# Kernel optimization log

Measured on AMD Instinct MI355X. Metric: run time of the kernel, lower is better.

Reference implementation:

```python
import jax, jax.numpy as jnp
import numpy as np

N_WIRES = 14
N_LAYERS = 3
DIM = 2 ** N_WIRES
BATCH = 1024


def _rx(theta):
    # RX(t) = [[cos t/2, -i sin t/2], [-i sin t/2, cos t/2]]
    c = jnp.cos(theta / 2).astype(jnp.complex64)
    s = jnp.sin(theta / 2).astype(jnp.complex64)
    return jnp.stack([jnp.stack([c, -1j * s]), jnp.stack([-1j * s, c])])


def _ry(theta):
    # RY(t) = [[cos t/2, -sin t/2], [sin t/2, cos t/2]]
    c = jnp.cos(theta / 2).astype(jnp.complex64)
    s = jnp.sin(theta / 2).astype(jnp.complex64)
    return jnp.stack([jnp.stack([c, -s]), jnp.stack([s, c])])


def _apply_1q(psi, U, w):
    # psi: (B, 2, 2, ..., 2); apply 2x2 U on qubit axis w+1
    psi = jnp.tensordot(psi, U, axes=((w + 1,), (1,)))  # contracted axis moves to end
    return jnp.moveaxis(psi, -1, w + 1)


def _apply_cnot(psi, c, t):
    # control qubit c, target qubit t (Python ints)
    a0 = jax.lax.index_in_dim(psi, 0, axis=c + 1, keepdims=True)
    a1 = jax.lax.index_in_dim(psi, 1, axis=c + 1, keepdims=True)
    a1 = jnp.flip(a1, axis=t + 1)  # X on target within control=1 subspace
    return jnp.concatenate([a0, a1], axis=c + 1)


def _circuit_features(state, params):
    # state: (B, 2**n) real normalized amplitudes -> PauliZ expvals (B, n)
    n = N_WIRES
    psi = state.astype(jnp.complex64).reshape((-1,) + (2,) * n)
    for layer in range(N_LAYERS):
        for w in range(n):
            psi = _apply_1q(psi, _rx(params[layer, w, 0]), w)
            psi = _apply_1q(psi, _ry(params[layer, w, 1]), w)
        for w in range(n - 1):
            psi = _apply_cnot(psi, w, w + 1)
        psi = _apply_cnot(psi, n - 1, 0)
    probs = jnp.real(psi * jnp.conj(psi))  # (B, 2, ..., 2)
    feats = []
    for w in range(n):
        axes = tuple(a for a in range(1, n + 1) if a != w + 1)
        p = jnp.sum(probs, axis=axes)  # (B, 2)
        feats.append(p[:, 0] - p[:, 1])  # <Z_w>
    return jnp.stack(feats, axis=1)  # (B, n)


def setup_inputs() -> dict:
    key = jax.random.key(0)
    k1, k2, k3 = jax.random.split(key, 3)
    state = jax.random.normal(k1, (BATCH, DIM), dtype=jnp.float32)
    state = state / jnp.linalg.norm(state, axis=1, keepdims=True)  # valid statevectors
    params = jax.random.normal(k2, (N_LAYERS, N_WIRES, 2), dtype=jnp.float32)
    head_w = jax.random.normal(k3, (1, N_WIRES), dtype=jnp.float32) * (1.0 / np.sqrt(N_WIRES))
    head_b = jnp.zeros((1,), dtype=jnp.float32)
    return {"state": state, "params": params, "head_w": head_w, "head_b": head_b}


def reference(state, params, head_w, head_b):
    feats = _circuit_features(state, params)          # (B, n_wires)
    out = feats @ head_w.T + head_b                   # (B, 1)
    return out[:, 0]                                  # (B,)
```

## Files before the change

### kernel.cpp

```cpp
#include <hip/hip_runtime.h>
#include <utility>

#define NW 14
#define NL 3
#define DIM 16384
#define NG  (NL * NW)
#define TPB 1024
#define MAXSP 12

typedef float v2f __attribute__((ext_vector_type(2)));

struct SP {
    int J = 0, nr = 0, nl = 0;
    unsigned dirs[4]  = {};
    unsigned traw[10] = {};
    unsigned tR[10] = {}, tW[10] = {};
    unsigned sxR[16] = {}, sxW[16] = {};
    unsigned pv[8]   = {};
    unsigned cpar[8] = {};
    unsigned gid[8]  = {};
    int wflag = 1;
};
struct Sched2 {
    int nsp = 0;
    SP sp[MAXSP] = {};
    unsigned stA[10] = {};
    unsigned stK[4]  = {};
    unsigned pz[NW]  = {};
    unsigned nib[NW] = {};
    int ok = 1;
};

constexpr unsigned fap(const unsigned* g, unsigned x) {
    unsigned r = 0;
    for (int b = 4; b < 14; ++b) if ((x >> b) & 1u) r ^= g[b - 4];
    return x ^ r;
}
constexpr int rank4n(const unsigned* v) {
    unsigned bas[4] = {}; int nb = 0;
    for (int i = 0; i < 4; ++i) {
        unsigned r = v[i] & 15u;
        for (int j = 0; j < nb; ++j) {
            int hb = 3; while (hb > 0 && !((bas[j] >> hb) & 1u)) --hb;
            if ((r >> hb) & 1u) r ^= bas[j];
        }
        if (r) bas[nb++] = r;
    }
    return nb;
}

constexpr Sched2 build2() {
    Sched2 S{};
    unsigned mk[NG] = {}, vmg[NG] = {}, zm[NW] = {};
    {
        unsigned A[NW] = {};
        for (int w = 0; w < NW; ++w) A[w] = 1u << (NW - 1 - w);
        int g = 0;
        for (int l = 0; l < NL; ++l) {
            unsigned rows[NW] = {};
            for (int u = 0; u < NW; ++u) rows[u] = A[u] | (1u << (NW + u));
            for (int col = 0; col < NW; ++col) {
                int piv = col;
                while (piv < NW && !((rows[piv] >> col) & 1u)) ++piv;
                if (piv >= NW) { S.ok = 0; continue; }
                unsigned tmp = rows[col]; rows[col] = rows[piv]; rows[piv] = tmp;
                for (int r = 0; r < NW; ++r)
                    if (r != col && ((rows[r] >> col) & 1u)) rows[r] ^= rows[col];
            }
            for (int w = 0; w < NW; ++w) {
                unsigned m = 0;
                for (int r = 0; r < NW; ++r) m |= ((rows[r] >> (NW + w)) & 1u) << r;
                mk[g] = m; vmg[g] = A[w]; ++g;
            }
            for (int w = 0; w < NW - 1; ++w) A[w + 1] ^= A[w];
            A[0] ^= A[NW - 1];
        }
        for (int w = 0; w < NW; ++w) zm[w] = A[w];
    }
    int gs = 0;
    while (gs < NG && S.nsp < MAXSP) {
        SP& P = S.sp[S.nsp];
        unsigned bas[14] = {}; int nb = 0;
        int j = gs;
        while (j < NG && (j - gs) < 8) {
            unsigned r = mk[j];
            for (int i = 0; i < nb; ++i) {
                int hb = 13; while (hb > 0 && !((bas[i] >> hb) & 1u)) --hb;
                if ((r >> hb) & 1u) r ^= bas[i];
            }
            if (!r) break;
            bas[nb++] = r; ++j;
        }
        P.J = j - gs; P.nr = P.J < 4 ? P.J : 4; P.nl = P.J - P.nr;
        for (int q = 0; q < P.J; ++q) P.gid[q] = (unsigned)(gs + q);
        for (int q = 0; q < P.nr; ++q) P.dirs[q] = mk[gs + q];
        for (int q = P.nr; q < 4; ++q) {
            for (int b = 0; b < NW; ++b) {
                unsigned r = 1u << b;
                for (int i = 0; i < nb; ++i) {
                    int hb = 13; while (hb > 0 && !((bas[i] >> hb) & 1u)) --hb;
                    if ((r >> hb) & 1u) r ^= bas[i];
                }
                if (r) { bas[nb++] = r; P.dirs[q] = 1u << b; break; }
            }
        }
        unsigned lm[4] = {};
        for (int i = 0; i < P.nl; ++i) lm[i] = mk[gs + 4 + i];
        unsigned tt[4] = { 0, 0, 0, 0 };
        if (P.nl > 0) tt[0] = lm[0];
        if (P.nl > 1) tt[1] = lm[1];
        if (P.nl > 2) tt[2] = lm[2] ^ tt[0] ^ tt[1];
        if (P.nl > 3) tt[3] = lm[3] ^ lm[2];
        for (int i = P.nl; i < 4; ++i) {
            for (int b = 0; b < NW; ++b) {
                unsigned r = 1u << b;
                for (int k2 = 0; k2 < nb; ++k2) {
                    int hb = 13; while (hb > 0 && !((bas[k2] >> hb) & 1u)) --hb;
                    if ((r >> hb) & 1u) r ^= bas[k2];
                }
                if (r) { bas[nb++] = r; tt[i] = 1u << b; break; }
            }
        }
        for (int i = 0; i < 4; ++i) P.traw[i] = tt[i];
        for (int b6 = 4; b6 < 10; ++b6) {
            for (int b = 0; b < NW; ++b) {
                unsigned r = 1u << b;
                for (int k2 = 0; k2 < nb; ++k2) {
                    int hb = 13; while (hb > 0 && !((bas[k2] >> hb) & 1u)) --hb;
                    if ((r >> hb) & 1u) r ^= bas[k2];
                }
                if (r) { bas[nb++] = r; P.traw[b6] = 1u << b; break; }
            }
        }
        if (nb != 14) S.ok = 0;
        for (int q = 0; q < P.J; ++q) {
            unsigned vm = vmg[gs + q], p = 0;
            for (int b = 0; b < 10; ++b)
                if (__builtin_popcount(P.traw[b] & vm) & 1) p |= 1u << b;
            P.pv[q] = p;
            unsigned cp = 0;
            for (int s = 0; s < 16; ++s) {
                unsigned sx = 0;
                for (int q2 = 0; q2 < 4; ++q2) if ((s >> q2) & 1) sx ^= P.dirs[q2];
                if (__builtin_popcount(sx & vm) & 1) cp |= 1u << s;
            }
            P.cpar[q] = cp;
        }
        ++S.nsp; gs = j;
    }
    if (gs < NG) S.ok = 0;
    S.sp[S.nsp - 1].wflag = 0;
    for (int t = 0; t < S.nsp; ++t) {
        unsigned wd[4] = {}, rd[4] = {};
        if (t == 0) { wd[0] = 4; wd[1] = 8; wd[2] = 16; wd[3] = 32; }
        else for (int i = 0; i < 4; ++i) wd[i] = S.sp[t - 1].traw[i];
        for (int i = 0; i < 4; ++i) rd[i] = S.sp[t].traw[i];
        unsigned bg[10] = {}; int bscore = -1;
        for (unsigned seed = 0; seed < 512u; ++seed) {
            unsigned g[10] = {};
            if (seed) {
                for (int b = 0; b < 10; ++b) {
                    unsigned h = (seed * 2654435761u) ^ ((unsigned)(b + 3) * 0x9E3779B9u);
                    h ^= h >> 16; h *= 2246822519u; h ^= h >> 13;
                    g[b] = h & 15u;
                }
            }
            unsigned W[4] = {}, R[4] = {};
            for (int i = 0; i < 4; ++i) { W[i] = fap(g, wd[i]); R[i] = fap(g, rd[i]); }
            int sc = rank4n(W) + rank4n(R);
            if (sc > bscore) {
                bscore = sc;
                for (int b = 0; b < 10; ++b) bg[b] = g[b];
                if (sc == 8) break;
            }
        }
        for (int b = 0; b < 10; ++b) S.sp[t].tR[b] = fap(bg, S.sp[t].traw[b]);
        for (int s = 0; s < 16; ++s) {
            unsigned sx = 0;
            for (int q = 0; q < 4; ++q) if ((s >> q) & 1) sx ^= S.sp[t].dirs[q];
            S.sp[t].sxR[s] = fap(bg, sx);
        }
        if (t == 0) {
            for (int b = 0; b < 10; ++b) S.stA[b] = fap(bg, 4u << b);
            for (int k = 0; k < 4; ++k) S.stK[k] = fap(bg, (unsigned)k << 12);
        } else {
            for (int b = 0; b < 10; ++b) S.sp[t - 1].tW[b] = fap(bg, S.sp[t - 1].traw[b]);
            for (int s = 0; s < 16; ++s) {
                unsigned sx = 0;
                for (int q = 0; q < 4; ++q) if ((s >> q) & 1) sx ^= S.sp[t - 1].dirs[q];
                S.sp[t - 1].sxW[s] = fap(bg, sx);
            }
        }
    }
    for (int w = 0; w < NW; ++w) {
        const SP& L = S.sp[S.nsp - 1];
        unsigned p = 0;
        for (int b = 0; b < 10; ++b)
            if (__builtin_popcount(L.traw[b] & zm[w]) & 1) p |= 1u << b;
        S.pz[w] = p;
        unsigned nv = 0;
        for (int q = 0; q < 4; ++q)
            if (__builtin_popcount(L.dirs[q] & zm[w]) & 1) nv |= 1u << q;
        S.nib[w] = nv;
    }
    return S;
}
constexpr Sched2 SC2 = build2();
static_assert(SC2.ok == 1, "schedule build failed");
static_assert(SC2.nsp <= MAXSP, "too many superphases");

template<class F, unsigned... I>
__device__ __forceinline__ void static_for_impl(F&& f, std::integer_sequence<unsigned, I...>) {
    (f(std::integral_constant<unsigned, I>{}), ...);
}
template<unsigned N, class F>
__device__ __forceinline__ void static_for(F&& f) {
    static_for_impl(static_cast<F&&>(f), std::make_integer_sequence<unsigned, N>{});
}

template<int NEGLO, int NEGHI>
__device__ __forceinline__ v2f cmul(v2f k, v2f x) {
    v2f y;
    if constexpr (!NEGLO)
        asm("v_pk_mul_f32 %0, %1, %2 op_sel:[0,0] op_sel_hi:[0,1]"
            : "=&v"(y) : "v"(k), "v"(x));
    else
        asm("v_pk_mul_f32 %0, %1, %2 op_sel:[0,0] op_sel_hi:[0,1] neg_lo:[1,0] neg_hi:[1,0]"
            : "=&v"(y) : "v"(k), "v"(x));
    if constexpr (!NEGHI)
        asm("v_pk_fma_f32 %0, %1, %2, %0 op_sel:[1,1,0] op_sel_hi:[1,0,1] neg_lo:[0,1,0]"
            : "+v"(y) : "v"(k), "v"(x));
    else
        asm("v_pk_fma_f32 %0, %1, %2, %0 op_sel:[1,1,0] op_sel_hi:[1,0,1] neg_lo:[1,1,0] neg_hi:[1,0,0]"
            : "+v"(y) : "v"(k), "v"(x));
    return y;
}
template<int NEGLO, int NEGHI>
__device__ __forceinline__ void cmac(v2f& y, v2f k, v2f x) {
    if constexpr (!NEGLO)
        asm("v_pk_fma_f32 %0, %1, %2, %0 op_sel:[0,0,0] op_sel_hi:[0,1,1]"
            : "+v"(y) : "v"(k), "v"(x));
    else
        asm("v_pk_fma_f32 %0, %1, %2, %0 op_sel:[0,0,0] op_sel_hi:[0,1,1] neg_lo:[1,0,0] neg_hi:[1,0,0]"
            : "+v"(y) : "v"(k), "v"(x));
    if constexpr (!NEGHI)
        asm("v_pk_fma_f32 %0, %1, %2, %0 op_sel:[1,1,0] op_sel_hi:[1,0,1] neg_lo:[0,1,0]"
            : "+v"(y) : "v"(k), "v"(x));
    else
        asm("v_pk_fma_f32 %0, %1, %2, %0 op_sel:[1,1,0] op_sel_hi:[1,0,1] neg_lo:[1,1,0] neg_hi:[1,0,0]"
            : "+v"(y) : "v"(k), "v"(x));
}
template<bool CS> __device__ __forceinline__ v2f  cmulA(v2f k, v2f x) { return cmul<0, CS ? 1 : 0>(k, x); }
template<bool CS> __device__ __forceinline__ void cmacB(v2f& y, v2f k, v2f x) { cmac<CS ? 1 : 0, 0>(y, k, x); }

constexpr int lane_ctrl(int li) {
    return li == 0 ? 0xB1 : li == 1 ? 0x4E : li == 2 ? 0x141 : 0x140;
}
template<int CTRL>
__device__ __forceinline__ v2f dppx(v2f x) {
    int lo = __builtin_amdgcn_update_dpp(0, __float_as_int(x.x), CTRL, 0xf, 0xf, false);
    int hi = __builtin_amdgcn_update_dpp(0, __float_as_int(x.y), CTRL, 0xf, 0xf, false);
    return (v2f){ __int_as_float(lo), __int_as_float(hi) };
}

template<int PIDX>
__device__ __forceinline__ void apply_sp(char* psiB, const float4* __restrict__ umat,
                                         unsigned tid, v2f* x)
{
    unsigned frep = 0;
    static_for<10>([&](auto Bc) {
        constexpr int b = (int)decltype(Bc)::value;
        constexpr unsigned mm = SC2.sp[PIDX].tR[b] |
                                (SC2.sp[PIDX].wflag ? (SC2.sp[PIDX].tW[b] << 16) : 0u);
        frep ^= mm & (unsigned)(-(int)((tid >> b) & 1u));
    });
    const unsigned srepR8 = (frep & 0x3FFFu) << 3;
    const unsigned srepW8 = ((frep >> 16) & 0x3FFFu) << 3;

    static_for<16>([&](auto Sc) {
        constexpr unsigned s = decltype(Sc)::value;
        constexpr unsigned off = SC2.sp[PIDX].sxR[s] << 3;
        x[s] = *(const v2f*)(psiB + (srepR8 ^ off));
    });
    if constexpr (SC2.sp[PIDX].wflag)
        __syncthreads();

    static_for<8>([&](auto Qc) {
        constexpr int q = (int)decltype(Qc)::value;
        if constexpr (q < SC2.sp[PIDX].J) {
            constexpr unsigned cp = SC2.sp[PIDX].cpar[q];
            constexpr unsigned pv = SC2.sp[PIDX].pv[q];
            const float4 u = umat[SC2.sp[PIDX].gid[q]];
            const unsigned sm = ((unsigned)__popc(tid & pv)) << 31;
            v2f A, B;
            A.x = u.x; A.y = __uint_as_float(__float_as_uint(u.y) ^ sm);
            B.x = __uint_as_float(__float_as_uint(u.z) ^ sm); B.y = u.w;
            if constexpr (q < SC2.sp[PIDX].nr) {
                static_for<8>([&](auto Pc) {
                    constexpr unsigned p    = decltype(Pc)::value;
                    constexpr unsigned lowm = (1u << q) - 1u;
                    constexpr unsigned s0   = ((p & ~lowm) << 1) | (p & lowm);
                    constexpr unsigned s1   = s0 | (1u << q);
                    constexpr bool c0 = (cp >> s0) & 1u;
                    constexpr bool c1 = (cp >> s1) & 1u;
                    const v2f x0 = x[s0], x1 = x[s1];
                    v2f y0 = cmulA<c0>(A, x0); cmacB<c0>(y0, B, x1);
                    v2f y1 = cmulA<c1>(A, x1); cmacB<c1>(y1, B, x0);
                    x[s0] = y0; x[s1] = y1;
                });
            } else {
                constexpr int ctrl = lane_ctrl(q - SC2.sp[PIDX].nr);
                static_for<16>([&](auto Sc) {
                    constexpr unsigned s = decltype(Sc)::value;
                    constexpr bool cs = (cp >> s) & 1u;
                    v2f recv = dppx<ctrl>(x[s]);
                    v2f y = cmulA<cs>(A, x[s]); cmacB<cs>(y, B, recv);
                    x[s] = y;
                });
            }
        }
    });

    if constexpr (SC2.sp[PIDX].wflag) {
        static_for<16>([&](auto Sc) {
            constexpr unsigned s = decltype(Sc)::value;
            constexpr unsigned off = SC2.sp[PIDX].sxW[s] << 3;
            *(v2f*)(psiB + (srepW8 ^ off)) = x[s];
        });
        __syncthreads();
    }
}

__global__ __launch_bounds__(TPB) void qsim_kernel(
    const float* __restrict__ state,
    const float* __restrict__ params,
    const float* __restrict__ head_w,
    const float* __restrict__ head_b,
    float* __restrict__ out)
{
    __shared__ v2f    psi[DIM];
    __shared__ float4 umat[NG];
    __shared__ float  red[TPB / 64];
    char* psiB = (char*)psi;
    const unsigned tid = threadIdx.x;

    if (tid < NG) {
        float t1 = 0.5f * params[2 * tid + 0];
        float t2 = 0.5f * params[2 * tid + 1];
        float s1, c1, s2, c2;
        sincosf(t1, &s1, &c1);
        sincosf(t2, &s2, &c2);
        umat[tid] = make_float4(c1 * c2, s1 * s2, -s2 * c1, -c2 * s1);
    }

    unsigned tpart = 0;
    static_for<10>([&](auto Bc) {
        constexpr int b = (int)decltype(Bc)::value;
        constexpr unsigned m = SC2.stA[b];
        tpart ^= m & (unsigned)(-(int)((tid >> b) & 1u));
    });
    const float4* st4 = reinterpret_cast<const float4*>(state) + (size_t)blockIdx.x * (DIM / 4);
    static_for<4>([&](auto Kc) {
        constexpr int k = (int)decltype(Kc)::value;
        float4 v = st4[tid + k * TPB];
        const unsigned bb = (tpart ^ SC2.stK[k]) << 3;
        *(v2f*)(psiB + (bb ^ (0u << 3))) = (v2f){ v.x, 0.f };
        *(v2f*)(psiB + (bb ^ (1u << 3))) = (v2f){ v.y, 0.f };
        *(v2f*)(psiB + (bb ^ (2u << 3))) = (v2f){ v.z, 0.f };
        *(v2f*)(psiB + (bb ^ (3u << 3))) = (v2f){ v.w, 0.f };
    });
    __syncthreads();

    v2f x[16];
    static_for<MAXSP>([&](auto Pc) {
        constexpr int p = (int)decltype(Pc)::value;
        if constexpr (p < SC2.nsp) apply_sp<p>(psiB, umat, tid, x);
    });

    float e[NW];
    static_for<NW>([&](auto Wc) {
        constexpr int w = (int)decltype(Wc)::value;
        constexpr unsigned pzw = SC2.pz[w];
        float hw = head_w[w];
        e[w] = (__popc(tid & pzw) & 1) ? -hw : hw;
    });
    float c[16];
    static_for<16>([&](auto Mc) { c[decltype(Mc)::value] = 0.f; });
    static_for<NW>([&](auto Wc) {
        constexpr int w = (int)decltype(Wc)::value;
        c[SC2.nib[w]] += e[w];
    });
    static_for<4>([&](auto Bc) {
        constexpr unsigned B = 1u << decltype(Bc)::value;
        static_for<16>([&](auto Kc) {
            constexpr unsigned k = decltype(Kc)::value;
            if constexpr (!(k & B)) {
                float a = c[k], b = c[k | B];
                c[k] = a + b; c[k | B] = a - b;
            }
        });
    });
    float acc = 0.f;
    static_for<16>([&](auto Sc) {
        constexpr int s = (int)decltype(Sc)::value;
        acc += (x[s].x * x[s].x + x[s].y * x[s].y) * c[s];
    });

#pragma unroll
    for (int off = 32; off > 0; off >>= 1)
        acc += __shfl_down(acc, off, 64);
    const unsigned lane = tid & 63, wv = tid >> 6;
    if (lane == 0) red[wv] = acc;
    __syncthreads();
    if (tid == 0) {
        float tot = 0.f;
#pragma unroll
        for (int i = 0; i < TPB / 64; ++i) tot += red[i];
        out[blockIdx.x] = tot + head_b[0];
    }
}

extern "C" void kernel_launch(void* const* d_in, const int* in_sizes, int n_in,
                              void* d_out, int out_size, void* d_ws, size_t ws_size,
                              hipStream_t stream) {
    const float* state  = (const float*)d_in[0];
    const float* params = (const float*)d_in[1];
    const float* head_w = (const float*)d_in[2];
    const float* head_b = (const float*)d_in[3];
    float* out = (float*)d_out;

    qsim_kernel<<<out_size, TPB, 0, stream>>>(state, params, head_w, head_b, out);
}
```

Before: 157.9 us.

## Replace superphase schedule with fixed 11-phase wave-private shared-memory permutation scheme

Rebuilds the compile-time schedule so each phase applies 4 gates in registers, with the basis split into 6 lane bits, 4 register bits and 4 fixed wave-local bits. The cross-lane DPP gate path is dropped. Reads use a simple contiguous per-wave address, and writes go through a computed XOR permutation. Because the fixed wave bits keep some phases' data inside a wave, barriers are only needed every other phase, cutting __syncthreads count. In exchange it runs more phases with more shared-memory round trips, and the write pattern may cause LDS bank conflicts.

```diff
diff --git a/kernel.cpp b/kernel.cpp
--- a/kernel.cpp
+++ b/kernel.cpp
@@ -6,51 +6,60 @@
 #define DIM 16384
 #define NG  (NL * NW)
 #define TPB 1024
-#define MAXSP 12
+#define NPH3 11
 
 typedef float v2f __attribute__((ext_vector_type(2)));
 
-struct SP {
-    int J = 0, nr = 0, nl = 0;
-    unsigned dirs[4]  = {};
-    unsigned traw[10] = {};
-    unsigned tR[10] = {}, tW[10] = {};
-    unsigned sxR[16] = {}, sxW[16] = {};
-    unsigned pv[8]   = {};
-    unsigned cpar[8] = {};
-    unsigned gid[8]  = {};
-    int wflag = 1;
+struct S3 {
+    int ok = 1;
+    unsigned Lane[NPH3][6] = {};
+    unsigned Reg[NPH3][4]  = {};
+    unsigned Vw[4]         = {};
+    unsigned WT[NPH3][6]   = {};
+    unsigned WS[NPH3][16]  = {};
+    unsigned pv[NPH3][4]   = {};
+    unsigned cp[NPH3][4]   = {};
+    unsigned ST[10] = {}, STK[4] = {}, STJ[4] = {};
+    unsigned pz[NW] = {}, nib[NW] = {};
 };
-struct Sched2 {
-    int nsp = 0;
-    SP sp[MAXSP] = {};
-    unsigned stA[10] = {};
-    unsigned stK[4]  = {};
-    unsigned pz[NW]  = {};
-    unsigned nib[NW] = {};
-    int ok = 1;
-};
-
-constexpr unsigned fap(const unsigned* g, unsigned x) {
-    unsigned r = 0;
-    for (int b = 4; b < 14; ++b) if ((x >> b) & 1u) r ^= g[b - 4];
-    return x ^ r;
-}
-constexpr int rank4n(const unsigned* v) {
-    unsigned bas[4] = {}; int nb = 0;
-    for (int i = 0; i < 4; ++i) {
-        unsigned r = v[i] & 15u;
-        for (int j = 0; j < nb; ++j) {
-            int hb = 3; while (hb > 0 && !((bas[j] >> hb) & 1u)) --hb;
-            if ((r >> hb) & 1u) r ^= bas[j];
-        }
-        if (r) bas[nb++] = r;
-    }
-    return nb;
-}
-
-constexpr Sched2 build2() {
-    Sched2 S{};
+
+constexpr int rank14(const unsigned* v, int n) {
+    unsigned piv[14] = {};
+    int r = 0;
+    for (int i = 0; i < n; ++i) {
+        unsigned x = v[i];
+        for (int bit = 13; bit >= 0; --bit) {
+            if (!((x >> bit) & 1u)) continue;
+            if (piv[bit]) { x ^= piv[bit]; }
+            else { piv[bit] = x; ++r; x = 0; break; }
+        }
+    }
+    return r;
+}
+
+constexpr unsigned coords14(const unsigned bas[14], unsigned v, int& ok) {
+    unsigned pv14[14] = {}, pc14[14] = {};
+    for (int b = 0; b < 14; ++b) {
+        unsigned x = bas[b], c = 1u << b;
+        for (int bit = 13; bit >= 0; --bit) {
+            if (!((x >> bit) & 1u)) continue;
+            if (pv14[bit]) { x ^= pv14[bit]; c ^= pc14[bit]; }
+            else { pv14[bit] = x; pc14[bit] = c; x = 0; break; }
+        }
+        if (x) ok = 0;
+    }
+    unsigned x = v, c = 0;
+    for (int bit = 13; bit >= 0; --bit) {
+        if ((x >> bit) & 1u) {
+            if (!pv14[bit]) { ok = 0; return 0; }
+            x ^= pv14[bit]; c ^= pc14[bit];
+        }
+    }
+    return c;
+}
+
+constexpr S3 build3() {
+    S3 S{};
     unsigned mk[NG] = {}, vmg[NG] = {}, zm[NW] = {};
     {
         unsigned A[NW] = {};
@@ -77,137 +86,173 @@
         }
         for (int w = 0; w < NW; ++w) zm[w] = A[w];
     }
-    int gs = 0;
-    while (gs < NG && S.nsp < MAXSP) {
-        SP& P = S.sp[S.nsp];
+    for (int p = 0; p < NPH3; ++p) {
+        int J = (p < 10) ? 4 : 2;
+        for (int q = 0; q < J; ++q) S.Reg[p][q] = mk[4 * p + q];
+    }
+    {
+        int found = 0;
+        for (unsigned seed = 1; seed < 256u && !found; ++seed) {
+            unsigned cand[4] = {};
+            for (int i = 0; i < 4; ++i) {
+                unsigned h = (seed * 2654435761u) ^ ((unsigned)(i + 1) * 0x9E3779B9u);
+                h ^= h >> 15; h *= 2246822519u; h ^= h >> 13; h *= 3266489917u; h ^= h >> 16;
+                cand[i] = h & 0x3FFFu;
+            }
+            if (rank14(cand, 4) != 4) continue;
+            int good = 1;
+            for (int g = 0; g < 6 && good; ++g) {
+                int nm = (g < 5) ? 8 : 2;
+                unsigned set[12] = {}; int n = 0;
+                for (int i = 0; i < nm; ++i) set[n++] = mk[8 * g + i];
+                for (int i = 0; i < 4; ++i) set[n++] = cand[i];
+                if (rank14(set, n) != n) good = 0;
+            }
+            if (good) { for (int i = 0; i < 4; ++i) S.Vw[i] = cand[i]; found = 1; }
+        }
+        if (!found) S.ok = 0;
+    }
+    for (int g = 0; g < 6; ++g) {
+        int nm = (g < 5) ? 8 : 2;
         unsigned bas[14] = {}; int nb = 0;
-        int j = gs;
-        while (j < NG && (j - gs) < 8) {
-            unsigned r = mk[j];
-            for (int i = 0; i < nb; ++i) {
-                int hb = 13; while (hb > 0 && !((bas[i] >> hb) & 1u)) --hb;
-                if ((r >> hb) & 1u) r ^= bas[i];
-            }
-            if (!r) break;
-            bas[nb++] = r; ++j;
-        }
-        P.J = j - gs; P.nr = P.J < 4 ? P.J : 4; P.nl = P.J - P.nr;
-        for (int q = 0; q < P.J; ++q) P.gid[q] = (unsigned)(gs + q);
-        for (int q = 0; q < P.nr; ++q) P.dirs[q] = mk[gs + q];
-        for (int q = P.nr; q < 4; ++q) {
-            for (int b = 0; b < NW; ++b) {
-                unsigned r = 1u << b;
-                for (int i = 0; i < nb; ++i) {
-                    int hb = 13; while (hb > 0 && !((bas[i] >> hb) & 1u)) --hb;
-                    if ((r >> hb) & 1u) r ^= bas[i];
+        for (int i = 0; i < 4; ++i) bas[nb++] = S.Vw[i];
+        for (int i = 0; i < nm; ++i) bas[nb++] = mk[8 * g + i];
+        unsigned fill[12] = {}; int nf = 0;
+        for (int b = 0; b < 14 && nb < 14; ++b) {
+            unsigned t[15] = {};
+            for (int i = 0; i < nb; ++i) t[i] = bas[i];
+            t[nb] = 1u << b;
+            if (rank14(t, nb + 1) == nb + 1) { bas[nb++] = 1u << b; fill[nf++] = 1u << b; }
+        }
+        if (nb != 14) S.ok = 0;
+        if (g < 5) {
+            int pA = 2 * g, pB = 2 * g + 1;
+            for (int b = 0; b < 4; ++b) { S.Lane[pA][b] = S.Reg[pB][b]; S.Lane[pB][b] = S.Reg[pA][b]; }
+            S.Lane[pA][4] = fill[0]; S.Lane[pA][5] = fill[1];
+            S.Lane[pB][4] = fill[0]; S.Lane[pB][5] = fill[1];
+        } else {
+            S.Reg[10][2] = fill[0]; S.Reg[10][3] = fill[1];
+            for (int b = 0; b < 6; ++b) S.Lane[10][b] = fill[2 + b];
+        }
+    }
+    for (int t = NPH3 - 2; t >= 0; --t) {
+        unsigned bas[14] = {};
+        for (int b = 0; b < 6; ++b) bas[b] = S.Lane[t + 1][b];
+        for (int q = 0; q < 4; ++q) bas[6 + q] = S.Reg[t + 1][q];
+        for (int j = 0; j < 4; ++j) bas[10 + j] = S.Vw[j];
+        unsigned rb[4] = {}; int rn = 0;
+        for (int b = 0; b < 6; ++b) {
+            int bestcs = 0, bestg = -1; unsigned bestr = 0;
+            for (int cs = 0; cs < 16; ++cs) {
+                unsigned c = 0;
+                for (int q = 0; q < 4; ++q) if ((cs >> q) & 1) c ^= S.Reg[t][q];
+                int ok2 = 1;
+                unsigned r = coords14(bas, S.Lane[t][b] ^ c, ok2) & 15u;
+                if (!ok2) continue;
+                unsigned x = r;
+                for (int i = 0; i < rn; ++i) {
+                    int hb = 3; while (hb > 0 && !((rb[i] >> hb) & 1u)) --hb;
+                    if ((x >> hb) & 1u) x ^= rb[i];
                 }
-                if (r) { bas[nb++] = r; P.dirs[q] = 1u << b; break; }
-            }
-        }
-        unsigned lm[4] = {};
-        for (int i = 0; i < P.nl; ++i) lm[i] = mk[gs + 4 + i];
-        unsigned tt[4] = { 0, 0, 0, 0 };
-        if (P.nl > 0) tt[0] = lm[0];
-        if (P.nl > 1) tt[1] = lm[1];
-        if (P.nl > 2) tt[2] = lm[2] ^ tt[0] ^ tt[1];
-        if (P.nl > 3) tt[3] = lm[3] ^ lm[2];
-        for (int i = P.nl; i < 4; ++i) {
-            for (int b = 0; b < NW; ++b) {
-                unsigned r = 1u << b;
-                for (int k2 = 0; k2 < nb; ++k2) {
-                    int hb = 13; while (hb > 0 && !((bas[k2] >> hb) & 1u)) --hb;
-                    if ((r >> hb) & 1u) r ^= bas[k2];
-                }
-                if (r) { bas[nb++] = r; tt[i] = 1u << b; break; }
-            }
-        }
-        for (int i = 0; i < 4; ++i) P.traw[i] = tt[i];
-        for (int b6 = 4; b6 < 10; ++b6) {
-            for (int b = 0; b < NW; ++b) {
-                unsigned r = 1u << b;
-                for (int k2 = 0; k2 < nb; ++k2) {
-                    int hb = 13; while (hb > 0 && !((bas[k2] >> hb) & 1u)) --hb;
-                    if ((r >> hb) & 1u) r ^= bas[k2];
-                }
-                if (r) { bas[nb++] = r; P.traw[b6] = 1u << b; break; }
-            }
-        }
-        if (nb != 14) S.ok = 0;
-        for (int q = 0; q < P.J; ++q) {
-            unsigned vm = vmg[gs + q], p = 0;
-            for (int b = 0; b < 10; ++b)
-                if (__builtin_popcount(P.traw[b] & vm) & 1) p |= 1u << b;
-            P.pv[q] = p;
-            unsigned cp = 0;
+                int gain = x ? 1 : 0;
+                if (gain > bestg) { bestg = gain; bestcs = cs; bestr = r; }
+                if (gain == 1) break;
+            }
+            unsigned c = 0;
+            for (int q = 0; q < 4; ++q) if ((bestcs >> q) & 1) c ^= S.Reg[t][q];
+            S.Lane[t][b] ^= c;
+            unsigned x = bestr;
+            for (int i = 0; i < rn; ++i) {
+                int hb = 3; while (hb > 0 && !((rb[i] >> hb) & 1u)) --hb;
+                if ((x >> hb) & 1u) x ^= rb[i];
+            }
+            if (x && rn < 4) rb[rn++] = x;
+        }
+        int okc = 1;
+        for (int b = 0; b < 6; ++b) S.WT[t][b] = coords14(bas, S.Lane[t][b], okc);
+        for (int s = 0; s < 16; ++s) {
+            unsigned v = 0;
+            for (int q = 0; q < 4; ++q) if ((s >> q) & 1) v ^= S.Reg[t][q];
+            S.WS[t][s] = coords14(bas, v, okc);
+        }
+        if (!okc) S.ok = 0;
+        if ((t & 1) == 0) {
+            for (int b = 0; b < 6; ++b) if (S.WT[t][b] >> 10) S.ok = 0;
+            for (int s = 0; s < 16; ++s) if (S.WS[t][s] >> 10) S.ok = 0;
+        }
+        for (int ub = 0; ub < 10; ++ub) {
+            unsigned wamp = (ub < 6) ? S.Lane[t][ub] : S.Vw[ub - 6];
+            unsigned widx = (ub < 6) ? S.WT[t][ub] : (1u << (10 + ub - 6));
+            unsigned ramp = 0;
+            for (int b = 0; b < 6; ++b) if ((widx >> b) & 1u) ramp ^= S.Lane[t + 1][b];
+            for (int q = 0; q < 4; ++q) if ((widx >> (6 + q)) & 1u) ramp ^= S.Reg[t + 1][q];
+            for (int j = 0; j < 4; ++j) if ((widx >> (10 + j)) & 1u) ramp ^= S.Vw[j];
+            if (ramp != wamp) S.ok = 0;
+        }
+        for (int q = 0; q < 4; ++q) {
+            unsigned widx = S.WS[t][1u << q];
+            unsigned ramp = 0;
+            for (int b = 0; b < 6; ++b) if ((widx >> b) & 1u) ramp ^= S.Lane[t + 1][b];
+            for (int qq = 0; qq < 4; ++qq) if ((widx >> (6 + qq)) & 1u) ramp ^= S.Reg[t + 1][qq];
+            for (int j = 0; j < 4; ++j) if ((widx >> (10 + j)) & 1u) ramp ^= S.Vw[j];
+            if (ramp != S.Reg[t][q]) S.ok = 0;
+        }
+    }
+    for (int p = 0; p < NPH3; ++p) {
+        int J = (p < 10) ? 4 : 2;
+        for (int q = 0; q < J; ++q) {
+            unsigned vm = vmg[4 * p + q], pvm = 0;
+            for (int b = 0; b < 6; ++b)
+                if (__builtin_popcount(S.Lane[p][b] & vm) & 1) pvm |= 1u << b;
+            for (int j = 0; j < 4; ++j)
+                if (__builtin_popcount(S.Vw[j] & vm) & 1) pvm |= 1u << (6 + j);
+            S.pv[p][q] = pvm;
+            unsigned cpm = 0;
             for (int s = 0; s < 16; ++s) {
-                unsigned sx = 0;
-                for (int q2 = 0; q2 < 4; ++q2) if ((s >> q2) & 1) sx ^= P.dirs[q2];
-                if (__builtin_popcount(sx & vm) & 1) cp |= 1u << s;
-            }
-            P.cpar[q] = cp;
-        }
-        ++S.nsp; gs = j;
-    }
-    if (gs < NG) S.ok = 0;
-    S.sp[S.nsp - 1].wflag = 0;
-    for (int t = 0; t < S.nsp; ++t) {
-        unsigned wd[4] = {}, rd[4] = {};
-        if (t == 0) { wd[0] = 4; wd[1] = 8; wd[2] = 16; wd[3] = 32; }
-        else for (int i = 0; i < 4; ++i) wd[i] = S.sp[t - 1].traw[i];
-        for (int i = 0; i < 4; ++i) rd[i] = S.sp[t].traw[i];
-        unsigned bg[10] = {}; int bscore = -1;
-        for (unsigned seed = 0; seed < 512u; ++seed) {
-            unsigned g[10] = {};
-            if (seed) {
-                for (int b = 0; b < 10; ++b) {
-                    unsigned h = (seed * 2654435761u) ^ ((unsigned)(b + 3) * 0x9E3779B9u);
-                    h ^= h >> 16; h *= 2246822519u; h ^= h >> 13;
-                    g[b] = h & 15u;
-                }
-            }
-            unsigned W[4] = {}, R[4] = {};
-            for (int i = 0; i < 4; ++i) { W[i] = fap(g, wd[i]); R[i] = fap(g, rd[i]); }
-            int sc = rank4n(W) + rank4n(R);
-            if (sc > bscore) {
-                bscore = sc;
-                for (int b = 0; b < 10; ++b) bg[b] = g[b];
-                if (sc == 8) break;
-            }
-        }
-        for (int b = 0; b < 10; ++b) S.sp[t].tR[b] = fap(bg, S.sp[t].traw[b]);
-        for (int s = 0; s < 16; ++s) {
-            unsigned sx = 0;
-            for (int q = 0; q < 4; ++q) if ((s >> q) & 1) sx ^= S.sp[t].dirs[q];
-            S.sp[t].sxR[s] = fap(bg, sx);
-        }
-        if (t == 0) {
-            for (int b = 0; b < 10; ++b) S.stA[b] = fap(bg, 4u << b);
-            for (int k = 0; k < 4; ++k) S.stK[k] = fap(bg, (unsigned)k << 12);
-        } else {
-            for (int b = 0; b < 10; ++b) S.sp[t - 1].tW[b] = fap(bg, S.sp[t - 1].traw[b]);
-            for (int s = 0; s < 16; ++s) {
-                unsigned sx = 0;
-                for (int q = 0; q < 4; ++q) if ((s >> q) & 1) sx ^= S.sp[t - 1].dirs[q];
-                S.sp[t - 1].sxW[s] = fap(bg, sx);
-            }
+                unsigned v = 0;
+                for (int q2 = 0; q2 < 4; ++q2) if ((s >> q2) & 1) v ^= S.Reg[p][q2];
+                if (__builtin_popcount(v & vm) & 1) cpm |= 1u << s;
+            }
+            S.cp[p][q] = cpm;
+        }
+    }
+    {
+        unsigned bas[14] = {};
+        for (int b = 0; b < 6; ++b) bas[b] = S.Lane[0][b];
+        for (int q = 0; q < 4; ++q) bas[6 + q] = S.Reg[0][q];
+        for (int j = 0; j < 4; ++j) bas[10 + j] = S.Vw[j];
+        int okc = 1;
+        for (int b = 0; b < 10; ++b) S.ST[b] = coords14(bas, 1u << (b + 2), okc);
+        for (int k = 0; k < 4; ++k) S.STK[k] = coords14(bas, (unsigned)k << 12, okc);
+        for (int j = 0; j < 4; ++j) S.STJ[j] = coords14(bas, (unsigned)j, okc);
+        if (!okc) S.ok = 0;
+        for (int ub = 0; ub < 18; ++ub) {
+            unsigned amp = (ub < 10) ? (1u << (ub + 2))
+                         : (ub < 14) ? ((unsigned)(ub - 10) << 12) : (unsigned)(ub - 14);
+            unsigned widx = (ub < 10) ? S.ST[ub] : (ub < 14) ? S.STK[ub - 10] : S.STJ[ub - 14];
+            unsigned ramp = 0;
+            for (int b = 0; b < 6; ++b) if ((widx >> b) & 1u) ramp ^= S.Lane[0][b];
+            for (int q = 0; q < 4; ++q) if ((widx >> (6 + q)) & 1u) ramp ^= S.Reg[0][q];
+            for (int j = 0; j < 4; ++j) if ((widx >> (10 + j)) & 1u) ramp ^= S.Vw[j];
+            if (ramp != amp) S.ok = 0;
         }
     }
     for (int w = 0; w < NW; ++w) {
-        const SP& L = S.sp[S.nsp - 1];
-        unsigned p = 0;
-        for (int b = 0; b < 10; ++b)
-            if (__builtin_popcount(L.traw[b] & zm[w]) & 1) p |= 1u << b;
-        S.pz[w] = p;
+        unsigned pzm = 0;
+        for (int b = 0; b < 6; ++b)
+            if (__builtin_popcount(S.Lane[10][b] & zm[w]) & 1) pzm |= 1u << b;
+        for (int j = 0; j < 4; ++j)
+            if (__builtin_popcount(S.Vw[j] & zm[w]) & 1) pzm |= 1u << (6 + j);
+        S.pz[w] = pzm;
         unsigned nv = 0;
         for (int q = 0; q < 4; ++q)
-            if (__builtin_popcount(L.dirs[q] & zm[w]) & 1) nv |= 1u << q;
+            if (__builtin_popcount(S.Reg[10][q] & zm[w]) & 1) nv |= 1u << q;
         S.nib[w] = nv;
     }
     return S;
 }
-constexpr Sched2 SC2 = build2();
-static_assert(SC2.ok == 1, "schedule build failed");
-static_assert(SC2.nsp <= MAXSP, "too many superphases");
+constexpr S3 SC3 = build3();
+static_assert(SC3.ok == 1, "schedule build failed");
 
 template<class F, unsigned... I>
 __device__ __forceinline__ void static_for_impl(F&& f, std::integer_sequence<unsigned, I...>) {
@@ -252,84 +297,6 @@
 }
 template<bool CS> __device__ __forceinline__ v2f  cmulA(v2f k, v2f x) { return cmul<0, CS ? 1 : 0>(k, x); }
 template<bool CS> __device__ __forceinline__ void cmacB(v2f& y, v2f k, v2f x) { cmac<CS ? 1 : 0, 0>(y, k, x); }
-
-constexpr int lane_ctrl(int li) {
-    return li == 0 ? 0xB1 : li == 1 ? 0x4E : li == 2 ? 0x141 : 0x140;
-}
-template<int CTRL>
-__device__ __forceinline__ v2f dppx(v2f x) {
-    int lo = __builtin_amdgcn_update_dpp(0, __float_as_int(x.x), CTRL, 0xf, 0xf, false);
-    int hi = __builtin_amdgcn_update_dpp(0, __float_as_int(x.y), CTRL, 0xf, 0xf, false);
-    return (v2f){ __int_as_float(lo), __int_as_float(hi) };
-}
-
-template<int PIDX>
-__device__ __forceinline__ void apply_sp(char* psiB, const float4* __restrict__ umat,
-                                         unsigned tid, v2f* x)
-{
-    unsigned frep = 0;
-    static_for<10>([&](auto Bc) {
-        constexpr int b = (int)decltype(Bc)::value;
-        constexpr unsigned mm = SC2.sp[PIDX].tR[b] |
-                                (SC2.sp[PIDX].wflag ? (SC2.sp[PIDX].tW[b] << 16) : 0u);
-        frep ^= mm & (unsigned)(-(int)((tid >> b) & 1u));
-    });
-    const unsigned srepR8 = (frep & 0x3FFFu) << 3;
-    const unsigned srepW8 = ((frep >> 16) & 0x3FFFu) << 3;
-
-    static_for<16>([&](auto Sc) {
-        constexpr unsigned s = decltype(Sc)::value;
-        constexpr unsigned off = SC2.sp[PIDX].sxR[s] << 3;
-        x[s] = *(const v2f*)(psiB + (srepR8 ^ off));
-    });
-    if constexpr (SC2.sp[PIDX].wflag)
-        __syncthreads();
-
-    static_for<8>([&](auto Qc) {
-        constexpr int q = (int)decltype(Qc)::value;
-        if constexpr (q < SC2.sp[PIDX].J) {
-            constexpr unsigned cp = SC2.sp[PIDX].cpar[q];
-            constexpr unsigned pv = SC2.sp[PIDX].pv[q];
-            const float4 u = umat[SC2.sp[PIDX].gid[q]];
-            const unsigned sm = ((unsigned)__popc(tid & pv)) << 31;
-            v2f A, B;
-            A.x = u.x; A.y = __uint_as_float(__float_as_uint(u.y) ^ sm);
-            B.x = __uint_as_float(__float_as_uint(u.z) ^ sm); B.y = u.w;
-            if constexpr (q < SC2.sp[PIDX].nr) {
-                static_for<8>([&](auto Pc) {
-                    constexpr unsigned p    = decltype(Pc)::value;
-                    constexpr unsigned lowm = (1u << q) - 1u;
-                    constexpr unsigned s0   = ((p & ~lowm) << 1) | (p & lowm);
-                    constexpr unsigned s1   = s0 | (1u << q);
-                    constexpr bool c0 = (cp >> s0) & 1u;
-                    constexpr bool c1 = (cp >> s1) & 1u;
-                    const v2f x0 = x[s0], x1 = x[s1];
-                    v2f y0 = cmulA<c0>(A, x0); cmacB<c0>(y0, B, x1);
-                    v2f y1 = cmulA<c1>(A, x1); cmacB<c1>(y1, B, x0);
-                    x[s0] = y0; x[s1] = y1;
-                });
-            } else {
-                constexpr int ctrl = lane_ctrl(q - SC2.sp[PIDX].nr);
-                static_for<16>([&](auto Sc) {
-                    constexpr unsigned s = decltype(Sc)::value;
-                    constexpr bool cs = (cp >> s) & 1u;
-                    v2f recv = dppx<ctrl>(x[s]);
-                    v2f y = cmulA<cs>(A, x[s]); cmacB<cs>(y, B, recv);
-                    x[s] = y;
-                });
-            }
-        }
-    });
-
-    if constexpr (SC2.sp[PIDX].wflag) {
-        static_for<16>([&](auto Sc) {
-            constexpr unsigned s = decltype(Sc)::value;
-            constexpr unsigned off = SC2.sp[PIDX].sxW[s] << 3;
-            *(v2f*)(psiB + (srepW8 ^ off)) = x[s];
-        });
-        __syncthreads();
-    }
-}
 
 __global__ __launch_bounds__(TPB) void qsim_kernel(
     const float* __restrict__ state,
@@ -353,34 +320,75 @@
         umat[tid] = make_float4(c1 * c2, s1 * s2, -s2 * c1, -c2 * s1);
     }
 
-    unsigned tpart = 0;
+    unsigned sidx = 0;
     static_for<10>([&](auto Bc) {
         constexpr int b = (int)decltype(Bc)::value;
-        constexpr unsigned m = SC2.stA[b];
-        tpart ^= m & (unsigned)(-(int)((tid >> b) & 1u));
+        sidx ^= SC3.ST[b] & (unsigned)(-(int)((tid >> b) & 1u));
     });
     const float4* st4 = reinterpret_cast<const float4*>(state) + (size_t)blockIdx.x * (DIM / 4);
     static_for<4>([&](auto Kc) {
         constexpr int k = (int)decltype(Kc)::value;
         float4 v = st4[tid + k * TPB];
-        const unsigned bb = (tpart ^ SC2.stK[k]) << 3;
-        *(v2f*)(psiB + (bb ^ (0u << 3))) = (v2f){ v.x, 0.f };
-        *(v2f*)(psiB + (bb ^ (1u << 3))) = (v2f){ v.y, 0.f };
-        *(v2f*)(psiB + (bb ^ (2u << 3))) = (v2f){ v.z, 0.f };
-        *(v2f*)(psiB + (bb ^ (3u << 3))) = (v2f){ v.w, 0.f };
+        const unsigned bi = sidx ^ SC3.STK[k];
+        *(v2f*)(psiB + ((bi ^ SC3.STJ[0]) << 3)) = (v2f){ v.x, 0.f };
+        *(v2f*)(psiB + ((bi ^ SC3.STJ[1]) << 3)) = (v2f){ v.y, 0.f };
+        *(v2f*)(psiB + ((bi ^ SC3.STJ[2]) << 3)) = (v2f){ v.z, 0.f };
+        *(v2f*)(psiB + ((bi ^ SC3.STJ[3]) << 3)) = (v2f){ v.w, 0.f };
     });
     __syncthreads();
 
+    const unsigned rbase = ((tid >> 6) << 13) | ((tid & 63u) << 3);
     v2f x[16];
-    static_for<MAXSP>([&](auto Pc) {
-        constexpr int p = (int)decltype(Pc)::value;
-        if constexpr (p < SC2.nsp) apply_sp<p>(psiB, umat, tid, x);
+
+    static_for<NPH3>([&](auto Pc) {
+        constexpr int P = (int)decltype(Pc)::value;
+        static_for<16>([&](auto Sc) {
+            constexpr int s = (int)decltype(Sc)::value;
+            x[s] = *(const v2f*)(psiB + rbase + (s << 9));
+        });
+        static_for<4>([&](auto Qc) {
+            constexpr int q = (int)decltype(Qc)::value;
+            if constexpr (q < ((P < 10) ? 4 : 2)) {
+                constexpr unsigned cp  = SC3.cp[P][q];
+                constexpr unsigned pvm = SC3.pv[P][q];
+                const float4 u = umat[4 * P + q];
+                const unsigned sm = ((unsigned)__popc(tid & pvm)) << 31;
+                v2f A, B;
+                A.x = u.x; A.y = __uint_as_float(__float_as_uint(u.y) ^ sm);
+                B.x = __uint_as_float(__float_as_uint(u.z) ^ sm); B.y = u.w;
+                static_for<8>([&](auto Pp) {
+                    constexpr unsigned pp   = decltype(Pp)::value;
+                    constexpr unsigned lowm = (1u << q) - 1u;
+                    constexpr unsigned s0   = ((pp & ~lowm) << 1) | (pp & lowm);
+                    constexpr unsigned s1   = s0 | (1u << q);
+                    constexpr bool c0 = (cp >> s0) & 1u;
+                    constexpr bool c1 = (cp >> s1) & 1u;
+                    const v2f x0 = x[s0], x1 = x[s1];
+                    v2f y0 = cmulA<c0>(A, x0); cmacB<c0>(y0, B, x1);
+                    v2f y1 = cmulA<c1>(A, x1); cmacB<c1>(y1, B, x0);
+                    x[s0] = y0; x[s1] = y1;
+                });
+            }
+        });
+        if constexpr (P < 10) {
+            if constexpr (P & 1) __syncthreads();
+            unsigned wi = (tid >> 6) << 10;
+            static_for<6>([&](auto Bc) {
+                constexpr int b = (int)decltype(Bc)::value;
+                wi ^= SC3.WT[P][b] & (unsigned)(-(int)((tid >> b) & 1u));
+            });
+            static_for<16>([&](auto Sc) {
+                constexpr int s = (int)decltype(Sc)::value;
+                *(v2f*)(psiB + ((wi ^ SC3.WS[P][s]) << 3)) = x[s];
+            });
+            if constexpr (P & 1) __syncthreads();
+        }
     });
 
     float e[NW];
     static_for<NW>([&](auto Wc) {
         constexpr int w = (int)decltype(Wc)::value;
-        constexpr unsigned pzw = SC2.pz[w];
+        constexpr unsigned pzw = SC3.pz[w];
         float hw = head_w[w];
         e[w] = (__popc(tid & pzw) & 1) ? -hw : hw;
     });
@@ -388,7 +396,7 @@
     static_for<16>([&](auto Mc) { c[decltype(Mc)::value] = 0.f; });
     static_for<NW>([&](auto Wc) {
         constexpr int w = (int)decltype(Wc)::value;
-        c[SC2.nib[w]] += e[w];
+        c[SC3.nib[w]] += e[w];
     });
     static_for<4>([&](auto Bc) {
         constexpr unsigned B = 1u << decltype(Bc)::value;
```

Result: faster. 133.6 us (-15.3%).
